# Performance work log

Measured on AMD Instinct MI355X. Metric: run time of the kernel, lower is better.

## Reference

```python
import jax, jax.numpy as jnp
import numpy as np

DIM_QK = 1024


def setup_inputs() -> dict:
    key = jax.random.key(0)
    ks = jax.random.split(key, 5)
    B, S, D = 4, 2048, 1024
    return {
        "x": jax.random.normal(ks[0], (B, S, D), dtype=jnp.float32),
        "Wq": jax.random.normal(ks[1], (DIM_QK, D), dtype=jnp.float32) * (D ** -0.5),
        "Wk": jax.random.normal(ks[2], (DIM_QK, D), dtype=jnp.float32) * (D ** -0.5),
        "Wv": jax.random.normal(ks[3], (D, D), dtype=jnp.float32) * (D ** -0.5),
        "Wo": jax.random.normal(ks[4], (D, D), dtype=jnp.float32) * (D ** -0.5),
    }


def reference(x, Wq, Wk, Wv, Wo):
    # torch Linear: y = x @ W.T (no bias)
    q = jnp.einsum('bsd,kd->bsk', x, Wq)
    k = jnp.einsum('bsd,kd->bsk', x, Wk)
    v = jnp.einsum('bsd,vd->bsv', x, Wv)
    scale = (DIM_QK // 2) ** (-0.5)
    dist = jnp.einsum('bqk,btk->bqt', q, k) * scale  # [B,S,S]
    weight = jax.lax.stop_gradient(dist)             # pre-softmax scores (detached)
    attn = jax.nn.softmax(dist, axis=-1)
    ctx = jnp.einsum('bqt,btv->bqv', attn, v)
    out = jnp.einsum('bqv,ev->bqe', ctx, Wo)
    return (out, weight)
```

## Files before the change

### kernel.cpp

```cpp
#include <hip/hip_runtime.h>
#include <stdint.h>

typedef __attribute__((ext_vector_type(8))) short bf16x8;
typedef __attribute__((ext_vector_type(4))) float f32x4;

__device__ __forceinline__ unsigned short f32_to_bf16(float f) {
  union { float f; unsigned int u; } v; v.f = f;
  unsigned int u = v.u;
  u += 0x7fffu + ((u >> 16) & 1u);
  return (unsigned short)(u >> 16);
}

__device__ __forceinline__ void gload_lds16(const unsigned short* g, unsigned short* lds_p) {
  __builtin_amdgcn_global_load_lds(
      (const __attribute__((address_space(1))) unsigned int*)g,
      (__attribute__((address_space(3))) unsigned int*)lds_p,
      16, 0, 0);
}


#define VM8  asm volatile("s_waitcnt vmcnt(8)" ::: "memory")
#define VM4  asm volatile("s_waitcnt vmcnt(4)" ::: "memory")
#define VM0_ asm volatile("s_waitcnt vmcnt(0)" ::: "memory")
#define VMNO ((void)0)

#define ISSUE_A(KT, KK) do {                                                  \
    const unsigned short* ga_ = As0 + (KT) * 64 + (KK) * 32;                  \
    unsigned short* la_ = &lds[(((KT) & 1) << 15) + (KK) * 8192 + t * 8];     \
    gload_lds16(ga_, la_);                                                    \
    gload_lds16(ga_ + a128, la_ + 4096);                                      \
  } while (0)

#define ISSUE_B(KT, KK) do {                                                  \
    const unsigned short* gb_ = Bs0 + (KT) * 64 + (KK) * 32;                  \
    unsigned short* lb_ = &lds[(((KT) & 1) << 15) + 16384 + (KK) * 8192 + t * 8]; \
    gload_lds16(gb_, lb_);                                                    \
    gload_lds16(gb_ + b128, lb_ + 4096);                                      \
  } while (0)

#define PH(BUFB, KK, MH, LOADB, ISSUE_CODE, VMC) do {                         \
    const int ab_ = (BUFB) + (KK) * 8192;                                     \
    if (LOADB) {                                                              \
      const int bb2_ = (BUFB) + 16384 + (KK) * 8192;                          \
      _Pragma("unroll")                                                       \
      for (int ni_ = 0; ni_ < 4; ++ni_)                                       \
        bfr[ni_] = *(const bf16x8*)&lds[bb2_ + (wc + ni_ * 16 + lrow) * 32 + q8e]; \
    }                                                                         \
    bf16x8 af_[4];                                                            \
    _Pragma("unroll")                                                         \
    for (int mi_ = 0; mi_ < 4; ++mi_)                                         \
      af_[mi_] = *(const bf16x8*)&lds[ab_ + (wr + (MH) * 64 + mi_ * 16 + lrow) * 32 + q8e]; \
    ISSUE_CODE;                                                               \
    __builtin_amdgcn_s_setprio(1);                                            \
    _Pragma("unroll")                                                         \
    for (int mi_ = 0; mi_ < 4; ++mi_) {                                       \
      _Pragma("unroll")                                                       \
      for (int ni_ = 0; ni_ < 4; ++ni_)                                       \
        acc[(MH) * 4 + mi_][ni_] = __builtin_amdgcn_mfma_f32_16x16x32_bf16(   \
            af_[mi_], bfr[ni_], acc[(MH) * 4 + mi_][ni_], 0, 0, 0);           \
    }                                                                         \
    __builtin_amdgcn_s_setprio(0);                                            \
    VMC;                                                                      \
    asm volatile("s_waitcnt lgkmcnt(0)" ::: "memory");                        \
    __builtin_amdgcn_s_barrier();                                             \
    asm volatile("" ::: "memory");                                            \
  } while (0)

template<int MODE>
__global__ __launch_bounds__(512, 2)
void gemm_bt(const unsigned short* __restrict__ A,
             const unsigned short* __restrict__ Bm,
             void* __restrict__ Cv,
             int M, int N, int K, int lda, int ldb, int ldc,
             long sA_, long sB_, long sC_,
             float scale)
{
  __shared__ unsigned short lds[65536];

  const int bz = blockIdx.z;
  const unsigned short* Ab = A + (long)bz * sA_;
  const unsigned short* Bb = Bm + (long)bz * sB_;

  const int m0 = blockIdx.x * 256;
  const int n0 = blockIdx.y * 256;

  const int t = threadIdx.x;
  const int lane = t & 63;
  const int w = t >> 6;
  const int wr = (w >> 2) * 128;
  const int wc = (w & 3) * 64;
  const int lrow = lane & 15;
  const int q8e = (lane >> 4) * 8;

  const int row0 = t >> 2;
  const int kc0 = (t & 3) * 8;
  const unsigned short* As0 = Ab + (long)(m0 + row0) * lda + kc0;
  const unsigned short* Bs0 = Bb + (long)(n0 + row0) * ldb + kc0;
  const long a128 = (long)lda * 128;
  const long b128 = (long)ldb * 128;

  f32x4 acc[8][4];
#pragma unroll
  for (int i = 0; i < 8; ++i)
#pragma unroll
    for (int j = 0; j < 4; ++j)
      acc[i][j] = (f32x4){0.f, 0.f, 0.f, 0.f};

  const int NT = K >> 6;

  ISSUE_A(0, 0); ISSUE_B(0, 0);
  ISSUE_A(0, 1); ISSUE_B(0, 1);
  ISSUE_A(1, 0); ISSUE_B(1, 0);
  VM8;
  __builtin_amdgcn_s_barrier();
  asm volatile("" ::: "memory");

  bf16x8 bfr[4];
  int kt = 0;
  for (; kt < NT - 2; ++kt) {
    const int bb = (kt & 1) << 15;
    PH(bb, 0, 0, 1, ISSUE_A(kt + 1, 1), VMNO);
    PH(bb, 0, 1, 0, ISSUE_B(kt + 1, 1), VM8);
    PH(bb, 1, 0, 1, ISSUE_A(kt + 2, 0), VMNO);
    PH(bb, 1, 1, 0, ISSUE_B(kt + 2, 0), VM8);
  }
  {
    const int bb = (kt & 1) << 15;
    PH(bb, 0, 0, 1, ISSUE_A(kt + 1, 1), VMNO);
    PH(bb, 0, 1, 0, ISSUE_B(kt + 1, 1), VM8);
    PH(bb, 1, 0, 1, VMNO, VMNO);
    PH(bb, 1, 1, 0, VMNO, VM4);
    ++kt;
  }
  {
    const int bb = (kt & 1) << 15;
    PH(bb, 0, 0, 1, VMNO, VMNO);
    PH(bb, 0, 1, 0, VMNO, VM0_);
    PH(bb, 1, 0, 1, VMNO, VMNO);
    PH(bb, 1, 1, 0, VMNO, VMNO);
  }

  const int cl = lane & 15;
  const int rq = (lane >> 4) * 4;

  if (MODE == 2) {
    float* Cb = (float*)Cv + (long)bz * sC_;
#pragma unroll
    for (int mig = 0; mig < 8; ++mig) {
      const int rowb = m0 + wr + (mig >> 2) * 64 + (mig & 3) * 16 + rq;
#pragma unroll
      for (int ni = 0; ni < 4; ++ni) {
        const int col = n0 + wc + ni * 16 + cl;
#pragma unroll
        for (int r = 0; r < 4; ++r)
          Cb[(long)(rowb + r) * ldc + col] = acc[mig][ni][r] * scale;
      }
    }
  } else {
    unsigned short* Cb = (unsigned short*)Cv + (long)bz * sC_;
#pragma unroll
    for (int mig = 0; mig < 8; ++mig) {
      const int rowb = m0 + wr + (mig >> 2) * 64 + (mig & 3) * 16 + rq;
#pragma unroll
      for (int ni = 0; ni < 4; ++ni) {
        const int col = n0 + wc + ni * 16 + cl;
#pragma unroll
        for (int r = 0; r < 4; ++r)
          Cb[(long)(rowb + r) * ldc + col] = f32_to_bf16(acc[mig][ni][r]);
      }
    }
  }
}

__global__ __launch_bounds__(256)
void softmax_rows(const float* __restrict__ dist, unsigned short* __restrict__ attn) {
  const long row = blockIdx.x;
  const float4* in = (const float4*)(dist + row * 2048);
  const int t = threadIdx.x;
  float4 v0 = in[t];
  float4 v1 = in[t + 256];

  float m = fmaxf(fmaxf(fmaxf(v0.x, v0.y), fmaxf(v0.z, v0.w)),
                  fmaxf(fmaxf(v1.x, v1.y), fmaxf(v1.z, v1.w)));
#pragma unroll
  for (int off = 32; off > 0; off >>= 1)
    m = fmaxf(m, __shfl_xor(m, off, 64));

  __shared__ float redm[4];
  __shared__ float reds[4];
  if ((t & 63) == 0) redm[t >> 6] = m;
  __syncthreads();
  m = fmaxf(fmaxf(redm[0], redm[1]), fmaxf(redm[2], redm[3]));

  float e[8];
  e[0] = __expf(v0.x - m); e[1] = __expf(v0.y - m);
  e[2] = __expf(v0.z - m); e[3] = __expf(v0.w - m);
  e[4] = __expf(v1.x - m); e[5] = __expf(v1.y - m);
  e[6] = __expf(v1.z - m); e[7] = __expf(v1.w - m);

  float s = ((e[0] + e[1]) + (e[2] + e[3])) + ((e[4] + e[5]) + (e[6] + e[7]));
#pragma unroll
  for (int off = 32; off > 0; off >>= 1)
    s += __shfl_xor(s, off, 64);
  if ((t & 63) == 0) reds[t >> 6] = s;
  __syncthreads();
  s = (reds[0] + reds[1]) + (reds[2] + reds[3]);

  const float inv = 1.0f / s;
  ushort4 o0, o1;
  o0.x = f32_to_bf16(e[0] * inv); o0.y = f32_to_bf16(e[1] * inv);
  o0.z = f32_to_bf16(e[2] * inv); o0.w = f32_to_bf16(e[3] * inv);
  o1.x = f32_to_bf16(e[4] * inv); o1.y = f32_to_bf16(e[5] * inv);
  o1.z = f32_to_bf16(e[6] * inv); o1.w = f32_to_bf16(e[7] * inv);
  *(ushort4*)(attn + row * 2048 + t * 4) = o0;
  *(ushort4*)(attn + row * 2048 + 1024 + t * 4) = o1;
}

__global__ __launch_bounds__(256)
void cast_all(const float* __restrict__ Wq, const float* __restrict__ Wk,
              const float* __restrict__ Wv, const float* __restrict__ Wo,
              const float* __restrict__ x, unsigned short* __restrict__ dst) {
  const long i = ((long)blockIdx.x * 256 + threadIdx.x) * 4;
  const float* src;
  long off;
  if (i < 4194304) {
    const int which = (int)(i >> 20);
    src = (which == 0) ? Wq : (which == 1) ? Wk : (which == 2) ? Wv : Wo;
    off = i & 1048575;
  } else {
    src = x;
    off = i - 4194304;
  }
  float4 v = *(const float4*)(src + off);
  ushort4 o;
  o.x = f32_to_bf16(v.x); o.y = f32_to_bf16(v.y);
  o.z = f32_to_bf16(v.z); o.w = f32_to_bf16(v.w);
  *(ushort4*)(dst + i) = o;
}

extern "C" void kernel_launch(void* const* d_in, const int* in_sizes, int n_in,
                              void* d_out, int out_size, void* d_ws, size_t ws_size,
                              hipStream_t stream) {
  const float* x  = (const float*)d_in[0];
  const float* Wq = (const float*)d_in[1];
  const float* Wk = (const float*)d_in[2];
  const float* Wv = (const float*)d_in[3];
  const float* Wo = (const float*)d_in[4];

  const long Bn = 4, S = 2048, D = 1024;
  const long MS = Bn * S;

  float* out_p  = (float*)d_out;
  float* weight = out_p + MS * D;

  unsigned short* Wqb = (unsigned short*)d_ws;
  unsigned short* Wvb = Wqb + 2 * D * D;
  unsigned short* Wob = Wvb + D * D;
  unsigned short* xb  = Wob + D * D;
  unsigned short* qk  = xb + MS * D;
  unsigned short* vtb = qk + MS * 2048;
  unsigned short* attn = qk;
  unsigned short* ctx  = xb;

  cast_all<<<12288, 256, 0, stream>>>(Wq, Wk, Wv, Wo, x, Wqb);

  gemm_bt<0><<<dim3(32, 8, 1), 512, 0, stream>>>(xb, Wqb, qk, 8192, 2048, 1024,
                                                 1024, 1024, 2048, 0, 0, 0, 1.f);
  gemm_bt<0><<<dim3(4, 8, 4), 512, 0, stream>>>(Wvb, xb, vtb, 1024, 2048, 1024,
                                                1024, 1024, 2048, 0, S * D, D * S, 1.f);
  gemm_bt<2><<<dim3(8, 8, 4), 512, 0, stream>>>(qk, qk + 1024, weight, 2048, 2048, 1024,
                                                2048, 2048, 2048,
                                                S * 2048, S * 2048, S * S,
                                                0.04419417382415922f);
  softmax_rows<<<(int)(Bn * S), 256, 0, stream>>>(weight, attn);
  gemm_bt<0><<<dim3(8, 4, 4), 512, 0, stream>>>(attn, vtb, ctx, 2048, 1024, 2048,
                                                2048, 2048, 1024,
                                                S * S, D * S, S * D, 1.f);
  gemm_bt<2><<<dim3(32, 4, 1), 512, 0, stream>>>(ctx, Wob, out_p, 8192, 1024, 1024,
                                                 1024, 1024, 1024, 0, 0, 0, 1.f);
}
```

Before: 346.9 us.

## Swizzle LDS layout and add 128x256 tile GEMM for small-grid launches

Applies an XOR swizzle to the k-chunk column used for global-to-LDS loads and for LDS fragment reads, intended to reduce LDS bank conflicts in both GEMM kernels. Adds a gemm_bt_128 variant with 128-row tiles and a smaller LDS footprint. The V-projection, attn@V and output-projection GEMMs use it, which doubles their block count so the 256 CUs are better filled. Smaller tiles give less data reuse per block and more total global traffic.

```diff
diff --git a/kernel.cpp b/kernel.cpp
--- a/kernel.cpp
+++ b/kernel.cpp
@@ -20,9 +20,12 @@
 
 
 #define VM8  asm volatile("s_waitcnt vmcnt(8)" ::: "memory")
+#define VM6  asm volatile("s_waitcnt vmcnt(6)" ::: "memory")
 #define VM4  asm volatile("s_waitcnt vmcnt(4)" ::: "memory")
+#define VM3  asm volatile("s_waitcnt vmcnt(3)" ::: "memory")
 #define VM0_ asm volatile("s_waitcnt vmcnt(0)" ::: "memory")
 #define VMNO ((void)0)
+
 
 #define ISSUE_A(KT, KK) do {                                                  \
     const unsigned short* ga_ = As0 + (KT) * 64 + (KK) * 32;                  \
@@ -44,12 +47,12 @@
       const int bb2_ = (BUFB) + 16384 + (KK) * 8192;                          \
       _Pragma("unroll")                                                       \
       for (int ni_ = 0; ni_ < 4; ++ni_)                                       \
-        bfr[ni_] = *(const bf16x8*)&lds[bb2_ + (wc + ni_ * 16 + lrow) * 32 + q8e]; \
+        bfr[ni_] = *(const bf16x8*)&lds[bb2_ + (wc + ni_ * 16 + lrow) * 32 + q8s]; \
     }                                                                         \
     bf16x8 af_[4];                                                            \
     _Pragma("unroll")                                                         \
     for (int mi_ = 0; mi_ < 4; ++mi_)                                         \
-      af_[mi_] = *(const bf16x8*)&lds[ab_ + (wr + (MH) * 64 + mi_ * 16 + lrow) * 32 + q8e]; \
+      af_[mi_] = *(const bf16x8*)&lds[ab_ + (wr + (MH) * 64 + mi_ * 16 + lrow) * 32 + q8s]; \
     ISSUE_CODE;                                                               \
     __builtin_amdgcn_s_setprio(1);                                            \
     _Pragma("unroll")                                                         \
@@ -90,10 +93,10 @@
   const int wr = (w >> 2) * 128;
   const int wc = (w & 3) * 64;
   const int lrow = lane & 15;
-  const int q8e = (lane >> 4) * 8;
+  const int q8s = (((lane >> 4) ^ ((lrow >> 1) & 3)) * 8);
 
   const int row0 = t >> 2;
-  const int kc0 = (t & 3) * 8;
+  const int kc0 = (((t & 3) ^ ((t >> 3) & 3)) * 8);
   const unsigned short* As0 = Ab + (long)(m0 + row0) * lda + kc0;
   const unsigned short* Bs0 = Bb + (long)(n0 + row0) * ldb + kc0;
   const long a128 = (long)lda * 128;
@@ -167,6 +170,142 @@
 #pragma unroll
         for (int r = 0; r < 4; ++r)
           Cb[(long)(rowb + r) * ldc + col] = f32_to_bf16(acc[mig][ni][r]);
+      }
+    }
+  }
+}
+
+
+#define ISSUE_A1(KT, KK) do {                                                 \
+    gload_lds16(As0 + (KT) * 64 + (KK) * 32,                                  \
+                &lds[((KT) & 1) * 24576 + (KK) * 4096 + t * 8]);              \
+  } while (0)
+
+#define ISSUE_B1(KT, KK) do {                                                 \
+    const unsigned short* gb_ = Bs0 + (KT) * 64 + (KK) * 32;                  \
+    unsigned short* lb_ = &lds[((KT) & 1) * 24576 + 8192 + (KK) * 8192 + t * 8]; \
+    gload_lds16(gb_, lb_);                                                    \
+    gload_lds16(gb_ + b128, lb_ + 4096);                                      \
+  } while (0)
+
+#define PH2(BUFB, KK, ISSUE_CODE, VMC) do {                                   \
+    const int ab_ = (BUFB) + (KK) * 4096;                                     \
+    const int bb_ = (BUFB) + 8192 + (KK) * 8192;                              \
+    bf16x8 af_[4], bf_[4];                                                    \
+    _Pragma("unroll")                                                         \
+    for (int i_ = 0; i_ < 4; ++i_) {                                          \
+      af_[i_] = *(const bf16x8*)&lds[ab_ + (wr + i_ * 16 + lrow) * 32 + q8s]; \
+      bf_[i_] = *(const bf16x8*)&lds[bb_ + (wc + i_ * 16 + lrow) * 32 + q8s]; \
+    }                                                                         \
+    ISSUE_CODE;                                                               \
+    __builtin_amdgcn_s_setprio(1);                                            \
+    _Pragma("unroll")                                                         \
+    for (int mi_ = 0; mi_ < 4; ++mi_) {                                       \
+      _Pragma("unroll")                                                       \
+      for (int ni_ = 0; ni_ < 4; ++ni_)                                       \
+        acc[mi_][ni_] = __builtin_amdgcn_mfma_f32_16x16x32_bf16(              \
+            af_[mi_], bf_[ni_], acc[mi_][ni_], 0, 0, 0);                      \
+    }                                                                         \
+    __builtin_amdgcn_s_setprio(0);                                            \
+    VMC;                                                                      \
+    asm volatile("s_waitcnt lgkmcnt(0)" ::: "memory");                        \
+    __builtin_amdgcn_s_barrier();                                             \
+    asm volatile("" ::: "memory");                                            \
+  } while (0)
+
+template<int MODE>
+__global__ __launch_bounds__(512, 2)
+void gemm_bt_128(const unsigned short* __restrict__ A,
+                 const unsigned short* __restrict__ Bm,
+                 void* __restrict__ Cv,
+                 int M, int N, int K, int lda, int ldb, int ldc,
+                 long sA_, long sB_, long sC_,
+                 float scale)
+{
+  __shared__ unsigned short lds[49152];
+
+  const int bz = blockIdx.z;
+  const unsigned short* Ab = A + (long)bz * sA_;
+  const unsigned short* Bb = Bm + (long)bz * sB_;
+
+  const int m0 = blockIdx.x * 128;
+  const int n0 = blockIdx.y * 256;
+
+  const int t = threadIdx.x;
+  const int lane = t & 63;
+  const int w = t >> 6;
+  const int wr = (w >> 2) * 64;
+  const int wc = (w & 3) * 64;
+  const int lrow = lane & 15;
+  const int q8s = (((lane >> 4) ^ ((lrow >> 1) & 3)) * 8);
+
+  const int row0 = t >> 2;
+  const int kc0 = (((t & 3) ^ ((t >> 3) & 3)) * 8);
+  const unsigned short* As0 = Ab + (long)(m0 + row0) * lda + kc0;
+  const unsigned short* Bs0 = Bb + (long)(n0 + row0) * ldb + kc0;
+  const long b128 = (long)ldb * 128;
+
+  f32x4 acc[4][4];
+#pragma unroll
+  for (int i = 0; i < 4; ++i)
+#pragma unroll
+    for (int j = 0; j < 4; ++j)
+      acc[i][j] = (f32x4){0.f, 0.f, 0.f, 0.f};
+
+  const int NT = K >> 6;
+
+  ISSUE_A1(0, 0); ISSUE_B1(0, 0);
+  ISSUE_A1(0, 1); ISSUE_B1(0, 1);
+  ISSUE_A1(1, 0); ISSUE_B1(1, 0);
+  VM6;
+  __builtin_amdgcn_s_barrier();
+  asm volatile("" ::: "memory");
+
+  int kt = 0;
+  for (; kt < NT - 2; ++kt) {
+    const int bb = (kt & 1) * 24576;
+    PH2(bb, 0, { ISSUE_A1(kt + 1, 1); ISSUE_B1(kt + 1, 1); }, VM6);
+    PH2(bb, 1, { ISSUE_A1(kt + 2, 0); ISSUE_B1(kt + 2, 0); }, VM6);
+  }
+  {
+    const int bb = (kt & 1) * 24576;
+    PH2(bb, 0, { ISSUE_A1(kt + 1, 1); ISSUE_B1(kt + 1, 1); }, VM6);
+    PH2(bb, 1, {}, VM3);
+    ++kt;
+  }
+  {
+    const int bb = (kt & 1) * 24576;
+    PH2(bb, 0, {}, VM0_);
+    PH2(bb, 1, {}, VMNO);
+  }
+
+  const int cl = lane & 15;
+  const int rq = (lane >> 4) * 4;
+
+  if (MODE == 2) {
+    float* Cb = (float*)Cv + (long)bz * sC_;
+#pragma unroll
+    for (int mi = 0; mi < 4; ++mi) {
+      const int rowb = m0 + wr + mi * 16 + rq;
+#pragma unroll
+      for (int ni = 0; ni < 4; ++ni) {
+        const int col = n0 + wc + ni * 16 + cl;
+#pragma unroll
+        for (int r = 0; r < 4; ++r)
+          Cb[(long)(rowb + r) * ldc + col] = acc[mi][ni][r] * scale;
+      }
+    }
+  } else {
+    unsigned short* Cb = (unsigned short*)Cv + (long)bz * sC_;
+#pragma unroll
+    for (int mi = 0; mi < 4; ++mi) {
+      const int rowb = m0 + wr + mi * 16 + rq;
+#pragma unroll
+      for (int ni = 0; ni < 4; ++ni) {
+        const int col = n0 + wc + ni * 16 + cl;
+#pragma unroll
+        for (int r = 0; r < 4; ++r)
+          Cb[(long)(rowb + r) * ldc + col] = f32_to_bf16(acc[mi][ni][r]);
       }
     }
   }
@@ -266,16 +405,16 @@
 
   gemm_bt<0><<<dim3(32, 8, 1), 512, 0, stream>>>(xb, Wqb, qk, 8192, 2048, 1024,
                                                  1024, 1024, 2048, 0, 0, 0, 1.f);
-  gemm_bt<0><<<dim3(4, 8, 4), 512, 0, stream>>>(Wvb, xb, vtb, 1024, 2048, 1024,
-                                                1024, 1024, 2048, 0, S * D, D * S, 1.f);
+  gemm_bt_128<0><<<dim3(8, 8, 4), 512, 0, stream>>>(Wvb, xb, vtb, 1024, 2048, 1024,
+                                                    1024, 1024, 2048, 0, S * D, D * S, 1.f);
   gemm_bt<2><<<dim3(8, 8, 4), 512, 0, stream>>>(qk, qk + 1024, weight, 2048, 2048, 1024,
                                                 2048, 2048, 2048,
                                                 S * 2048, S * 2048, S * S,
                                                 0.04419417382415922f);
   softmax_rows<<<(int)(Bn * S), 256, 0, stream>>>(weight, attn);
-  gemm_bt<0><<<dim3(8, 4, 4), 512, 0, stream>>>(attn, vtb, ctx, 2048, 1024, 2048,
-                                                2048, 2048, 1024,
-                                                S * S, D * S, S * D, 1.f);
-  gemm_bt<2><<<dim3(32, 4, 1), 512, 0, stream>>>(ctx, Wob, out_p, 8192, 1024, 1024,
-                                                 1024, 1024, 1024, 0, 0, 0, 1.f);
-}
+  gemm_bt_128<0><<<dim3(16, 4, 4), 512, 0, stream>>>(attn, vtb, ctx, 2048, 1024, 2048,
+                                                     2048, 2048, 1024,
+                                                     S * S, D * S, S * D, 1.f);
+  gemm_bt_128<2><<<dim3(64, 4, 1), 512, 0, stream>>>(ctx, Wob, out_p, 8192, 1024, 1024,
+                                                     1024, 1024, 1024, 0, 0, 0, 1.f);
+}
```

New measurement: 308.1 us. 11.2% less time.
